# Kernel tuning notes

Measured on AMD Instinct MI355X. Metric: run time of the kernel, lower is better.

Reference implementation:

```python
import jax, jax.numpy as jnp
import numpy as np

B, T, DIM, H, HD = 1, 4096, 1024, 8, 128
ATTN_SCALE = 0.12


def _rms_norm(x):
    # F.rms_norm with default eps = finfo(dtype).eps, no learned weight
    eps = jnp.asarray(jnp.finfo(x.dtype).eps, x.dtype)
    return x * jax.lax.rsqrt(jnp.mean(x * x, axis=-1, keepdims=True) + eps)


def _rotary(x):
    # x: [B, T, H, D]; half-rotary: last D/2 freqs are zero (identity)
    t, d = x.shape[1], x.shape[-1]
    freqs = (1.0 / 1024.0) ** jnp.linspace(0.0, 1.0, d // 4, dtype=jnp.float32)
    freqs = jnp.concatenate([freqs, jnp.zeros(d // 4, dtype=jnp.float32)])
    theta = jnp.arange(t, dtype=jnp.float32)[:, None] * freqs[None, :]  # [T, D/2]
    cos = jnp.cos(theta)[None, :, None, :]
    sin = jnp.sin(theta)[None, :, None, :]
    x1, x2 = jnp.split(x.astype(jnp.float32), 2, axis=-1)
    y = jnp.concatenate([x1 * cos + x2 * sin, -x1 * sin + x2 * cos], axis=-1)
    return y.astype(x.dtype)


def setup_inputs() -> dict:
    key = jax.random.key(0)
    k1, k2, k3, k4, k5 = jax.random.split(key, 5)
    std = 0.5 * DIM ** -0.5
    bound = (3.0 ** 0.5) * std
    x = jax.random.normal(k1, (B, T, DIM), dtype=jnp.float32)
    ve = jax.random.normal(k2, (B, T, DIM), dtype=jnp.float32)
    qkv_w = jax.random.uniform(k3, (3, H * HD, DIM), dtype=jnp.float32,
                               minval=-bound, maxval=bound)
    lambdas = jnp.array([0.5, 0.5], dtype=jnp.float32)
    # c_proj is zero-initialized in the source; use small random weights so the
    # output (and gradients) are non-trivial for correctness testing
    c_proj_w = jax.random.normal(k4, (DIM, H * HD), dtype=jnp.float32) * 0.02
    docs = jnp.sort(jax.random.randint(k5, (T,), 0, 8, dtype=jnp.int32))
    return {"x": x, "ve": ve, "qkv_w": qkv_w, "lambdas": lambdas,
            "c_proj_w": c_proj_w, "docs": docs}


def reference(x, ve, qkv_w, lambdas, c_proj_w, docs):
    b, t, _ = x.shape
    w = qkv_w.reshape(3 * H * HD, -1)              # [3*hdim, dim]
    qkv = (x @ w.T).reshape(b, t, 3, H, HD)        # chunk(3, dim=-2) == axis 2 here
    q, k, v = qkv[:, :, 0], qkv[:, :, 1], qkv[:, :, 2]
    q, k = _rms_norm(q), _rms_norm(k)
    q, k = _rotary(q), _rotary(k)
    v = lambdas[0] * v + lambdas[1] * ve.reshape(v.shape)
    # doc-causal mask: attend within the same document, causally
    i = jnp.arange(t)
    mask = (i[:, None] >= i[None, :]) & (docs[:, None] == docs[None, :])  # [T, T]
    scores = jnp.einsum('bihd,bjhd->bhij', q, k) * ATTN_SCALE
    scores = jnp.where(mask[None, None], scores, -jnp.inf)
    p = jax.nn.softmax(scores, axis=-1)
    y = jnp.einsum('bhij,bjhd->bihd', p, v).reshape(b, t, H * HD)
    return y @ c_proj_w.T
```

## Files before the change

### kernel.cpp

```cpp
#include <hip/hip_runtime.h>
#include <hip/hip_bf16.h>
#include <cstdint>

typedef __attribute__((ext_vector_type(8))) short sh8;
typedef __attribute__((ext_vector_type(4))) float f4;

#define T_SEQ 4096
#define DIMN  1024
#define NH    8
#define HDIM  128
#define NQKV  3072
#define ATTN_SCALE 0.12f

__device__ __forceinline__ ushort f2bf(float x) {
  __hip_bfloat16 b = __float2bfloat16(x);
  return *reinterpret_cast<ushort*>(&b);
}
__device__ __forceinline__ float bf2f(ushort u) {
  uint v = ((uint)u) << 16;
  float f;
  __builtin_memcpy(&f, &v, 4);
  return f;
}

#define GLDS16(g, l) \
  __builtin_amdgcn_global_load_lds((const __attribute__((address_space(1))) void*)(g), \
                                   (__attribute__((address_space(3))) void*)(l), 16, 0, 0)

__global__ void k_f32_to_bf16(const float* __restrict__ in, ushort* __restrict__ out, int n4) {
  int i = blockIdx.x * blockDim.x + threadIdx.x;
  if (i >= n4) return;
  float4 v = reinterpret_cast<const float4*>(in)[i];
  ushort4 o;
  o.x = f2bf(v.x); o.y = f2bf(v.y); o.z = f2bf(v.z); o.w = f2bf(v.w);
  reinterpret_cast<ushort4*>(out)[i] = o;
}

__global__ void k_docstart(const int* __restrict__ docs, int* __restrict__ dstart, int n) {
  int i = blockIdx.x * blockDim.x + threadIdx.x;
  if (i >= n) return;
  int d = docs[i];
  int lo = 0, hi = i;
  while (lo < hi) { int mid = (lo + hi) >> 1; if (docs[mid] < d) lo = mid + 1; else hi = mid; }
  dstart[i] = lo;
}

template <typename OT>
__global__ __launch_bounds__(256) void k_gemm(const ushort* __restrict__ A,
                                              const ushort* __restrict__ B,
                                              OT* __restrict__ C, int N, int K) {
  __shared__ ushort As[128 * 64];
  __shared__ ushort Bs[128 * 64];
  const int tid = threadIdx.x;
  const int lane = tid & 63;
  const int wave = tid >> 6;
  const int lr = lane & 15, lg = lane >> 4;
  const int wr = wave >> 1, wc = wave & 1;
  const int m0 = blockIdx.y * 128, n0 = blockIdx.x * 128;

  const f4 fzero = {0.f, 0.f, 0.f, 0.f};
  f4 acc[4][4];
#pragma unroll
  for (int i = 0; i < 4; ++i)
#pragma unroll
    for (int j = 0; j < 4; ++j) acc[i][j] = fzero;

  const int srow_base = wave * 8 + (lane >> 3);
  const int scg = lane & 7;

  for (int k0 = 0; k0 < K; k0 += 64) {
    __syncthreads();
#pragma unroll
    for (int i = 0; i < 4; ++i) {
      const int row = i * 32 + srow_base;
      const int cgl = scg ^ (row & 7);
      GLDS16(A + (size_t)(m0 + row) * K + k0 + cgl * 8, &As[i * 2048 + wave * 512]);
      GLDS16(B + (size_t)(n0 + row) * K + k0 + cgl * 8, &Bs[i * 2048 + wave * 512]);
    }
    __syncthreads();

#pragma unroll
    for (int kk = 0; kk < 2; ++kk) {
      sh8 af[4], bfv[4];
#pragma unroll
      for (int mt = 0; mt < 4; ++mt) {
        const int row = wr * 64 + mt * 16 + lr;
        af[mt] = *reinterpret_cast<const sh8*>(&As[row * 64 + (((kk * 4 + lg) ^ (row & 7)) * 8)]);
      }
#pragma unroll
      for (int nt = 0; nt < 4; ++nt) {
        const int row = wc * 64 + nt * 16 + lr;
        bfv[nt] = *reinterpret_cast<const sh8*>(&Bs[row * 64 + (((kk * 4 + lg) ^ (row & 7)) * 8)]);
      }
#pragma unroll
      for (int mt = 0; mt < 4; ++mt)
#pragma unroll
        for (int nt = 0; nt < 4; ++nt)
          acc[mt][nt] = __builtin_amdgcn_mfma_f32_16x16x32_bf16(af[mt], bfv[nt], acc[mt][nt], 0, 0, 0);
    }
  }

#pragma unroll
  for (int mt = 0; mt < 4; ++mt)
#pragma unroll
    for (int nt = 0; nt < 4; ++nt) {
      const int gcol = n0 + wc * 64 + nt * 16 + lr;
#pragma unroll
      for (int r = 0; r < 4; ++r) {
        const int grow = m0 + wr * 64 + mt * 16 + lg * 4 + r;
        float v = acc[mt][nt][r];
        if constexpr (sizeof(OT) == 2)
          C[(size_t)grow * N + gcol] = (OT)f2bf(v);
        else
          C[(size_t)grow * N + gcol] = (OT)v;
      }
    }
}

__global__ __launch_bounds__(64) void k_fuse(const ushort* __restrict__ qkvb,
                                             const float* __restrict__ ve,
                                             const float* __restrict__ lam,
                                             ushort* __restrict__ qh, ushort* __restrict__ kh,
                                             ushort* __restrict__ vh) {
  const int bid = blockIdx.x;
  const int t = bid >> 3, h = bid & 7;
  const int l = threadIdx.x;
  const ushort* base = qkvb + (size_t)t * NQKV + h * HDIM + 2 * l;
  uint qu = *reinterpret_cast<const uint*>(base);
  uint ku = *reinterpret_cast<const uint*>(base + 1024);
  uint vu = *reinterpret_cast<const uint*>(base + 2048);
  float q0 = bf2f((ushort)qu), q1 = bf2f((ushort)(qu >> 16));
  float k0 = bf2f((ushort)ku), k1 = bf2f((ushort)(ku >> 16));
  float v0 = bf2f((ushort)vu), v1 = bf2f((ushort)(vu >> 16));
  float sq = q0 * q0 + q1 * q1, sk = k0 * k0 + k1 * k1;
#pragma unroll
  for (int m = 1; m < 64; m <<= 1) { sq += __shfl_xor(sq, m); sk += __shfl_xor(sk, m); }
  const float eps = 1.1920928955078125e-07f;
  float rq = rsqrtf(sq * (1.f / 128.f) + eps);
  float rk = rsqrtf(sk * (1.f / 128.f) + eps);
  q0 *= rq; q1 *= rq; k0 *= rk; k1 *= rk;
  float c0 = 1.f, s0 = 0.f, c1 = 1.f, s1 = 0.f;
  if ((l & 31) < 16) {
    const int f0 = 2 * (l & 31);
    float fr0 = exp2f(-10.f * (float)f0 * (1.f / 31.f));
    float fr1 = exp2f(-10.f * (float)(f0 + 1) * (1.f / 31.f));
    sincosf((float)t * fr0, &s0, &c0);
    sincosf((float)t * fr1, &s1, &c1);
  }
  float qx0 = __shfl_xor(q0, 32), qx1 = __shfl_xor(q1, 32);
  float kx0 = __shfl_xor(k0, 32), kx1 = __shfl_xor(k1, 32);
  const float sgn = (l < 32) ? 1.f : -1.f;
  float qr0 = q0 * c0 + sgn * qx0 * s0;
  float qr1 = q1 * c1 + sgn * qx1 * s1;
  float kr0 = k0 * c0 + sgn * kx0 * s0;
  float kr1 = k1 * c1 + sgn * kx1 * s1;
  const float l0 = lam[0], l1 = lam[1];
  float2 vev = *reinterpret_cast<const float2*>(ve + (size_t)t * DIMN + h * HDIM + 2 * l);
  float vr0 = l0 * v0 + l1 * vev.x;
  float vr1 = l0 * v1 + l1 * vev.y;
  const size_t o = ((size_t)h * T_SEQ + t) * HDIM + 2 * l;
  *reinterpret_cast<uint*>(qh + o) = (uint)f2bf(qr0) | ((uint)f2bf(qr1) << 16);
  *reinterpret_cast<uint*>(kh + o) = (uint)f2bf(kr0) | ((uint)f2bf(kr1) << 16);
  *reinterpret_cast<uint*>(vh + o) = (uint)f2bf(vr0) | ((uint)f2bf(vr1) << 16);
}

__global__ __launch_bounds__(256) void k_vt(const ushort* __restrict__ vh, ushort* __restrict__ vt) {
  const int tb = blockIdx.x, db = blockIdx.y, h = blockIdx.z;
  __shared__ ushort L[64][68];
  const int tid = threadIdx.x;
  const int t0 = tb * 64, d0 = db * 64;
  const size_t ib = ((size_t)h * T_SEQ + t0) * HDIM + d0;
#pragma unroll
  for (int p = 0; p < 4; ++p) {
    const int row = p * 16 + (tid >> 4);
    const int c4 = (tid & 15) * 4;
    ushort4 v = *reinterpret_cast<const ushort4*>(vh + ib + (size_t)row * HDIM + c4);
    *reinterpret_cast<ushort4*>(&L[row][c4]) = v;
  }
  __syncthreads();
  const size_t ob = ((size_t)h * HDIM + d0) * T_SEQ + t0;
#pragma unroll
  for (int p = 0; p < 4; ++p) {
    const int drow = p * 16 + (tid >> 4);
    const int t4 = (tid & 15) * 4;
    ushort4 v;
    v.x = L[t4 + 0][drow]; v.y = L[t4 + 1][drow];
    v.z = L[t4 + 2][drow]; v.w = L[t4 + 3][drow];
    *reinterpret_cast<ushort4*>(vt + ob + (size_t)drow * T_SEQ + t4) = v;
  }
}

__global__ __launch_bounds__(256) void k_attn(const ushort* __restrict__ qh,
                                              const ushort* __restrict__ kh,
                                              const ushort* __restrict__ vt,
                                              const int* __restrict__ doc_start,
                                              ushort* __restrict__ y) {
  const int h  = blockIdx.x;
  const int qb = blockIdx.y;
  const int q0 = qb * 64;
  const int tid  = threadIdx.x;
  const int wave = tid >> 6;
  const int lane = tid & 63;
  const int lr = lane & 15, lg = lane >> 4;

  __shared__ ushort Ks[2][64 * 128];
  __shared__ ushort Vs[2][128 * 64];
  __shared__ ushort Ps[4][16 * 64];

  const ushort* Kg = kh + (size_t)h * T_SEQ * HDIM;
  const ushort* Vg = vt + (size_t)h * HDIM * T_SEQ;

  const int i_me = q0 + wave * 16 + lr;
  sh8 qf[4];
  {
    const ushort* qp = qh + ((size_t)h * T_SEQ + i_me) * HDIM + lg * 8;
#pragma unroll
    for (int c = 0; c < 4; ++c) qf[c] = *reinterpret_cast<const sh8*>(qp + c * 32);
  }
  const int ds_me = doc_start[i_me];
  const int ds_hi = doc_start[q0 + 63];
  const int kb0   = doc_start[q0] >> 6;

  const f4 fzero = {0.f, 0.f, 0.f, 0.f};
  f4 o_acc[8];
#pragma unroll
  for (int i = 0; i < 8; ++i) o_acc[i] = fzero;
  float m_me = -1e30f, l_me = 0.f;

  auto STAGE = [&](int b, int k0) {
#pragma unroll
    for (int p = 0; p < 4; ++p) {
      const int c = p * 256 + tid;
      const int row = c >> 4, cc = c & 15;
      GLDS16(Kg + (size_t)(k0 + row) * HDIM + (cc ^ (row & 7)) * 8,
             &Ks[b][(p * 256 + wave * 64) * 8]);
    }
#pragma unroll
    for (int p = 0; p < 4; ++p) {
      const int c = p * 256 + tid;
      const int d = c >> 3, cc = c & 7;
      GLDS16(Vg + (size_t)d * T_SEQ + k0 + (cc ^ (d & 7)) * 8,
             &Vs[b][(p * 256 + wave * 64) * 8]);
    }
  };

  int cur = 0;
  STAGE(0, kb0 * 64);

  const int sw = (lr & 7) << 4;

  for (int kb = kb0; kb <= qb; ++kb) {
    const int k0 = kb * 64;
    __syncthreads();
    if (kb < qb) STAGE(cur ^ 1, k0 + 64);

    const char* Kb = (const char*)&Ks[cur][0];
    const char* Vb = (const char*)&Vs[cur][0];
    char* Pw = (char*)&Ps[wave][0];

    f4 sacc[4];
#pragma unroll
    for (int jt = 0; jt < 4; ++jt) sacc[jt] = fzero;
#pragma unroll
    for (int jt = 0; jt < 4; ++jt)
#pragma unroll
      for (int c = 0; c < 4; ++c) {
        sh8 kf = *reinterpret_cast<const sh8*>(Kb + (jt * 16 + lr) * 256 + ((c * 64 + lg * 16) ^ sw));
        sacc[jt] = __builtin_amdgcn_mfma_f32_16x16x32_bf16(kf, qf[c], sacc[jt], 0, 0, 0);
      }

    const bool fullblk = (kb < qb) && (ds_hi <= k0);
    float p[4][4];
#pragma unroll
    for (int jt = 0; jt < 4; ++jt)
#pragma unroll
      for (int r = 0; r < 4; ++r) {
        float s = sacc[jt][r] * ATTN_SCALE;
        const int j = k0 + jt * 16 + lg * 4 + r;
        bool valid = fullblk || ((j <= i_me) && (j >= ds_me));
        p[jt][r] = valid ? s : -1e30f;
      }
    float tm = -1e30f;
#pragma unroll
    for (int jt = 0; jt < 4; ++jt) {
      float a = fmaxf(p[jt][0], p[jt][1]), b = fmaxf(p[jt][2], p[jt][3]);
      tm = fmaxf(tm, fmaxf(a, b));
    }
    tm = fmaxf(tm, __shfl_xor(tm, 16));
    tm = fmaxf(tm, __shfl_xor(tm, 32));
    const float mnew = fmaxf(m_me, tm);
    const float sc = __expf(m_me - mnew);
    m_me = mnew;
    float rs = 0.f;
#pragma unroll
    for (int jt = 0; jt < 4; ++jt)
#pragma unroll
      for (int r = 0; r < 4; ++r) {
        float pv = __expf(p[jt][r] - mnew);
        p[jt][r] = pv;
        rs += pv;
      }
    rs += __shfl_xor(rs, 16);
    rs += __shfl_xor(rs, 32);
    l_me = l_me * sc + rs;

#pragma unroll
    for (int jt = 0; jt < 4; ++jt) {
      uint2 u;
      u.x = (uint)f2bf(p[jt][0]) | ((uint)f2bf(p[jt][1]) << 16);
      u.y = (uint)f2bf(p[jt][2]) | ((uint)f2bf(p[jt][3]) << 16);
      *reinterpret_cast<uint2*>(Pw + lr * 128 + ((jt * 32 + lg * 8) ^ sw)) = u;
    }

    float sco[4];
#pragma unroll
    for (int rr = 0; rr < 4; ++rr) sco[rr] = __shfl(sc, lg * 4 + rr);
#pragma unroll
    for (int dt = 0; dt < 8; ++dt)
#pragma unroll
      for (int rr = 0; rr < 4; ++rr) o_acc[dt][rr] *= sco[rr];

#pragma unroll
    for (int ks = 0; ks < 2; ++ks) {
      sh8 pa = *reinterpret_cast<const sh8*>(Pw + lr * 128 + ((ks * 64 + lg * 16) ^ sw));
#pragma unroll
      for (int dt = 0; dt < 8; ++dt) {
        sh8 vf = *reinterpret_cast<const sh8*>(Vb + (dt * 16 + lr) * 128 + ((ks * 64 + lg * 16) ^ sw));
        o_acc[dt] = __builtin_amdgcn_mfma_f32_16x16x32_bf16(pa, vf, o_acc[dt], 0, 0, 0);
      }
    }

    __builtin_amdgcn_s_barrier();
    cur ^= 1;
  }

  float lo[4];
#pragma unroll
  for (int rr = 0; rr < 4; ++rr) lo[rr] = __shfl(l_me, lg * 4 + rr);
#pragma unroll
  for (int dt = 0; dt < 8; ++dt)
#pragma unroll
    for (int rr = 0; rr < 4; ++rr) {
      const int trow = q0 + wave * 16 + lg * 4 + rr;
      y[(size_t)trow * DIMN + h * HDIM + dt * 16 + lr] = f2bf(o_acc[dt][rr] / lo[rr]);
    }
}

extern "C" void kernel_launch(void* const* d_in, const int* in_sizes, int n_in,
                              void* d_out, int out_size, void* d_ws, size_t ws_size,
                              hipStream_t stream) {
  const float* x    = (const float*)d_in[0];
  const float* ve   = (const float*)d_in[1];
  const float* qkvw = (const float*)d_in[2];
  const float* lam  = (const float*)d_in[3];
  const float* cpw  = (const float*)d_in[4];
  const int*   docs = (const int*)d_in[5];
  float* out = (float*)d_out;
  char* ws = (char*)d_ws;

  ushort* qkvb = (ushort*)(ws);
  ushort* xb   = (ushort*)(ws + (24ull << 20));
  ushort* wb   = (ushort*)(ws + (32ull << 20));
  ushort* cb   = (ushort*)(ws + (38ull << 20));
  ushort* qh   = (ushort*)(ws + (40ull << 20));
  ushort* kh   = (ushort*)(ws + (48ull << 20));
  ushort* vh   = (ushort*)(ws + (56ull << 20));
  ushort* vt   = (ushort*)(ws + (64ull << 20));
  ushort* yb   = (ushort*)(ws + (72ull << 20));
  int*  dstart = (int*)(ws + (80ull << 20));

  k_f32_to_bf16<<<(T_SEQ * DIMN / 4) / 256, 256, 0, stream>>>(x, xb, T_SEQ * DIMN / 4);
  k_f32_to_bf16<<<(NQKV * DIMN / 4) / 256, 256, 0, stream>>>(qkvw, wb, NQKV * DIMN / 4);
  k_f32_to_bf16<<<(DIMN * DIMN / 4) / 256, 256, 0, stream>>>(cpw, cb, DIMN * DIMN / 4);

  k_gemm<ushort><<<dim3(NQKV / 128, T_SEQ / 128), 256, 0, stream>>>(xb, wb, qkvb, NQKV, DIMN);

  k_fuse<<<T_SEQ * NH, 64, 0, stream>>>(qkvb, ve, lam, qh, kh, vh);
  k_docstart<<<T_SEQ / 256, 256, 0, stream>>>(docs, dstart, T_SEQ);
  k_vt<<<dim3(T_SEQ / 64, HDIM / 64, NH), 256, 0, stream>>>(vh, vt);

  k_attn<<<dim3(NH, T_SEQ / 64), 256, 0, stream>>>(qh, kh, vt, dstart, yb);

  k_gemm<float><<<dim3(DIMN / 128, T_SEQ / 128), 256, 0, stream>>>(yb, cb, out, DIMN, DIMN);
}
```

Before: 117.9 us.

## Merge prep kernels, add triple-buffered GEMM with larger tiles, batch fuse blocks

```diff
diff --git a/kernel.cpp b/kernel.cpp
--- a/kernel.cpp
+++ b/kernel.cpp
@@ -27,104 +27,163 @@
   __builtin_amdgcn_global_load_lds((const __attribute__((address_space(1))) void*)(g), \
                                    (__attribute__((address_space(3))) void*)(l), 16, 0, 0)
 
-__global__ void k_f32_to_bf16(const float* __restrict__ in, ushort* __restrict__ out, int n4) {
-  int i = blockIdx.x * blockDim.x + threadIdx.x;
-  if (i >= n4) return;
-  float4 v = reinterpret_cast<const float4*>(in)[i];
-  ushort4 o;
-  o.x = f2bf(v.x); o.y = f2bf(v.y); o.z = f2bf(v.z); o.w = f2bf(v.w);
-  reinterpret_cast<ushort4*>(out)[i] = o;
-}
-
-__global__ void k_docstart(const int* __restrict__ docs, int* __restrict__ dstart, int n) {
-  int i = blockIdx.x * blockDim.x + threadIdx.x;
-  if (i >= n) return;
-  int d = docs[i];
-  int lo = 0, hi = i;
-  while (lo < hi) { int mid = (lo + hi) >> 1; if (docs[mid] < d) lo = mid + 1; else hi = mid; }
-  dstart[i] = lo;
-}
-
-template <typename OT>
-__global__ __launch_bounds__(256) void k_gemm(const ushort* __restrict__ A,
-                                              const ushort* __restrict__ B,
-                                              OT* __restrict__ C, int N, int K) {
-  __shared__ ushort As[128 * 64];
-  __shared__ ushort Bs[128 * 64];
+template <int N>
+__device__ __forceinline__ void wait_vmcnt() {
+  if constexpr (N == 0)      asm volatile("s_waitcnt vmcnt(0)" ::: "memory");
+  else if constexpr (N == 4) asm volatile("s_waitcnt vmcnt(4)" ::: "memory");
+  else if constexpr (N == 6) asm volatile("s_waitcnt vmcnt(6)" ::: "memory");
+  else if constexpr (N == 8) asm volatile("s_waitcnt vmcnt(8)" ::: "memory");
+  __builtin_amdgcn_sched_barrier(0);
+}
+
+__global__ __launch_bounds__(256) void k_prep(const float* __restrict__ x,
+                                              const float* __restrict__ qw,
+                                              const float* __restrict__ cw,
+                                              ushort* __restrict__ xb, ushort* __restrict__ wb,
+                                              ushort* __restrict__ cbuf,
+                                              const int* __restrict__ docs, int* __restrict__ dstart) {
+  const int b = blockIdx.x;
+  if (b < 8192) {
+    const int i = b * 256 + threadIdx.x;
+    const float* src;
+    ushort* dst;
+    int j;
+    if (i < 1048576)       { src = x;  dst = xb;   j = i; }
+    else if (i < 1835008)  { src = qw; dst = wb;   j = i - 1048576; }
+    else                   { src = cw; dst = cbuf; j = i - 1835008; }
+    float4 v = reinterpret_cast<const float4*>(src)[j];
+    ushort4 o;
+    o.x = f2bf(v.x); o.y = f2bf(v.y); o.z = f2bf(v.z); o.w = f2bf(v.w);
+    reinterpret_cast<ushort4*>(dst)[j] = o;
+  } else {
+    const int i = (b - 8192) * 256 + threadIdx.x;
+    if (i < T_SEQ) {
+      int d = docs[i];
+      int lo = 0, hi = i;
+      while (lo < hi) { int mid = (lo + hi) >> 1; if (docs[mid] < d) lo = mid + 1; else hi = mid; }
+      dstart[i] = lo;
+    }
+  }
+}
+
+template <int BM, int BN, int WM, int WN, typename OT>
+__global__ __launch_bounds__(WM * WN * 64) void k_gemm2(const ushort* __restrict__ A,
+                                                        const ushort* __restrict__ B,
+                                                        OT* __restrict__ C,
+                                                        int N, int K, int gx) {
+  constexpr int NW  = WM * WN;
+  constexpr int CHA = BM * 4;
+  constexpr int CHT = (BM + BN) * 4;
+  constexpr int LPW = CHT / (NW * 64);
+  constexpr int TILEB = (BM + BN) * 64;
+  constexpr int MF = BM / WM / 16;
+  constexpr int NF = BN / WN / 16;
+
+  __shared__ __attribute__((aligned(16))) char lds[3 * TILEB];
+
   const int tid = threadIdx.x;
   const int lane = tid & 63;
-  const int wave = tid >> 6;
+  const int w = tid >> 6;
   const int lr = lane & 15, lg = lane >> 4;
-  const int wr = wave >> 1, wc = wave & 1;
-  const int m0 = blockIdx.y * 128, n0 = blockIdx.x * 128;
+  const int wm = w / WN, wn = w % WN;
+
+  const int nwg = gridDim.x;
+  const int nb = (blockIdx.x & 7) * (nwg >> 3) + (blockIdx.x >> 3);
+  const int m0 = (nb / gx) * BM;
+  const int n0 = (nb % gx) * BN;
 
   const f4 fzero = {0.f, 0.f, 0.f, 0.f};
-  f4 acc[4][4];
-#pragma unroll
-  for (int i = 0; i < 4; ++i)
-#pragma unroll
-    for (int j = 0; j < 4; ++j) acc[i][j] = fzero;
-
-  const int srow_base = wave * 8 + (lane >> 3);
-  const int scg = lane & 7;
-
-  for (int k0 = 0; k0 < K; k0 += 64) {
-    __syncthreads();
-#pragma unroll
-    for (int i = 0; i < 4; ++i) {
-      const int row = i * 32 + srow_base;
-      const int cgl = scg ^ (row & 7);
-      GLDS16(A + (size_t)(m0 + row) * K + k0 + cgl * 8, &As[i * 2048 + wave * 512]);
-      GLDS16(B + (size_t)(n0 + row) * K + k0 + cgl * 8, &Bs[i * 2048 + wave * 512]);
-    }
-    __syncthreads();
-
-#pragma unroll
-    for (int kk = 0; kk < 2; ++kk) {
-      sh8 af[4], bfv[4];
-#pragma unroll
-      for (int mt = 0; mt < 4; ++mt) {
-        const int row = wr * 64 + mt * 16 + lr;
-        af[mt] = *reinterpret_cast<const sh8*>(&As[row * 64 + (((kk * 4 + lg) ^ (row & 7)) * 8)]);
-      }
-#pragma unroll
-      for (int nt = 0; nt < 4; ++nt) {
-        const int row = wc * 64 + nt * 16 + lr;
-        bfv[nt] = *reinterpret_cast<const sh8*>(&Bs[row * 64 + (((kk * 4 + lg) ^ (row & 7)) * 8)]);
-      }
-#pragma unroll
-      for (int mt = 0; mt < 4; ++mt)
-#pragma unroll
-        for (int nt = 0; nt < 4; ++nt)
-          acc[mt][nt] = __builtin_amdgcn_mfma_f32_16x16x32_bf16(af[mt], bfv[nt], acc[mt][nt], 0, 0, 0);
-    }
-  }
-
-#pragma unroll
-  for (int mt = 0; mt < 4; ++mt)
-#pragma unroll
-    for (int nt = 0; nt < 4; ++nt) {
-      const int gcol = n0 + wc * 64 + nt * 16 + lr;
+  f4 acc[MF][NF];
+#pragma unroll
+  for (int i = 0; i < MF; ++i)
+#pragma unroll
+    for (int j = 0; j < NF; ++j) acc[i][j] = fzero;
+
+  const int NT = K >> 5;
+
+  auto STAGE = [&](int t, int buf) {
+    const int k0 = t << 5;
+#pragma unroll
+    for (int l = 0; l < LPW; ++l) {
+      const int cb = (l * NW + w) * 64;
+      const int ch = cb + lane;
+      const ushort* src;
+      if (ch < CHA) {
+        const int row = ch >> 2;
+        const int cs = (ch & 3) ^ ((row >> 1) & 3);
+        src = A + (size_t)(m0 + row) * K + k0 + cs * 8;
+      } else {
+        const int c2 = ch - CHA;
+        const int row = c2 >> 2;
+        const int cs = (c2 & 3) ^ ((row >> 1) & 3);
+        src = B + (size_t)(n0 + row) * K + k0 + cs * 8;
+      }
+      GLDS16(src, lds + buf * TILEB + cb * 16);
+    }
+  };
+
+  STAGE(0, 0);
+  STAGE(1, 1);
+  wait_vmcnt<LPW>();
+  __builtin_amdgcn_s_barrier();
+
+  const int sw4 = (lr >> 1) & 3;
+  int bufc = 0;
+
+  for (int t = 0; t < NT; ++t) {
+    const bool more = (t + 2) < NT;
+    if (more) STAGE(t + 2, bufc == 0 ? 2 : (bufc == 1 ? 0 : 1));
+
+    const char* bb = lds + bufc * TILEB;
+    sh8 af[MF], bf[NF];
+#pragma unroll
+    for (int mt = 0; mt < MF; ++mt) {
+      const int row = wm * (BM / WM) + mt * 16 + lr;
+      af[mt] = *reinterpret_cast<const sh8*>(bb + (row * 4 + (lg ^ sw4)) * 16);
+    }
+#pragma unroll
+    for (int nt = 0; nt < NF; ++nt) {
+      const int row = wn * (BN / WN) + nt * 16 + lr;
+      bf[nt] = *reinterpret_cast<const sh8*>(bb + (CHA + row * 4 + (lg ^ sw4)) * 16);
+    }
+    __builtin_amdgcn_s_setprio(1);
+#pragma unroll
+    for (int mt = 0; mt < MF; ++mt)
+#pragma unroll
+      for (int nt = 0; nt < NF; ++nt)
+        acc[mt][nt] = __builtin_amdgcn_mfma_f32_16x16x32_bf16(af[mt], bf[nt], acc[mt][nt], 0, 0, 0);
+    __builtin_amdgcn_s_setprio(0);
+
+    if (more) wait_vmcnt<LPW>();
+    else      wait_vmcnt<0>();
+    __builtin_amdgcn_s_barrier();
+    bufc = bufc == 2 ? 0 : bufc + 1;
+  }
+
+#pragma unroll
+  for (int mt = 0; mt < MF; ++mt)
+#pragma unroll
+    for (int nt = 0; nt < NF; ++nt) {
+      const int gcol = n0 + wn * (BN / WN) + nt * 16 + lr;
 #pragma unroll
       for (int r = 0; r < 4; ++r) {
-        const int grow = m0 + wr * 64 + mt * 16 + lg * 4 + r;
-        float v = acc[mt][nt][r];
+        const int grow = m0 + wm * (BM / WM) + mt * 16 + lg * 4 + r;
         if constexpr (sizeof(OT) == 2)
-          C[(size_t)grow * N + gcol] = (OT)f2bf(v);
+          C[(size_t)grow * N + gcol] = (OT)f2bf(acc[mt][nt][r]);
         else
-          C[(size_t)grow * N + gcol] = (OT)v;
-      }
-    }
-}
-
-__global__ __launch_bounds__(64) void k_fuse(const ushort* __restrict__ qkvb,
-                                             const float* __restrict__ ve,
-                                             const float* __restrict__ lam,
-                                             ushort* __restrict__ qh, ushort* __restrict__ kh,
-                                             ushort* __restrict__ vh) {
-  const int bid = blockIdx.x;
-  const int t = bid >> 3, h = bid & 7;
-  const int l = threadIdx.x;
+          C[(size_t)grow * N + gcol] = (OT)acc[mt][nt][r];
+      }
+    }
+}
+
+__global__ __launch_bounds__(256) void k_fuse(const ushort* __restrict__ qkvb,
+                                              const float* __restrict__ ve,
+                                              const float* __restrict__ lam,
+                                              ushort* __restrict__ qh, ushort* __restrict__ kh,
+                                              ushort* __restrict__ vh) {
+  const int pair = blockIdx.x * 4 + (threadIdx.x >> 6);
+  const int t = pair >> 3, h = pair & 7;
+  const int l = threadIdx.x & 63;
   const ushort* base = qkvb + (size_t)t * NQKV + h * HDIM + 2 * l;
   uint qu = *reinterpret_cast<const uint*>(base);
   uint ku = *reinterpret_cast<const uint*>(base + 1024);
@@ -369,17 +428,14 @@
   ushort* yb   = (ushort*)(ws + (72ull << 20));
   int*  dstart = (int*)(ws + (80ull << 20));
 
-  k_f32_to_bf16<<<(T_SEQ * DIMN / 4) / 256, 256, 0, stream>>>(x, xb, T_SEQ * DIMN / 4);
-  k_f32_to_bf16<<<(NQKV * DIMN / 4) / 256, 256, 0, stream>>>(qkvw, wb, NQKV * DIMN / 4);
-  k_f32_to_bf16<<<(DIMN * DIMN / 4) / 256, 256, 0, stream>>>(cpw, cb, DIMN * DIMN / 4);
-
-  k_gemm<ushort><<<dim3(NQKV / 128, T_SEQ / 128), 256, 0, stream>>>(xb, wb, qkvb, NQKV, DIMN);
-
-  k_fuse<<<T_SEQ * NH, 64, 0, stream>>>(qkvb, ve, lam, qh, kh, vh);
-  k_docstart<<<T_SEQ / 256, 256, 0, stream>>>(docs, dstart, T_SEQ);
+  k_prep<<<8192 + 16, 256, 0, stream>>>(x, qkvw, cpw, xb, wb, cb, docs, dstart);
+
+  k_gemm2<256, 128, 2, 2, ushort><<<384, 256, 0, stream>>>(xb, wb, qkvb, NQKV, DIMN, NQKV / 128);
+
+  k_fuse<<<T_SEQ * NH / 4, 256, 0, stream>>>(qkvb, ve, lam, qh, kh, vh);
   k_vt<<<dim3(T_SEQ / 64, HDIM / 64, NH), 256, 0, stream>>>(vh, vt);
 
   k_attn<<<dim3(NH, T_SEQ / 64), 256, 0, stream>>>(qh, kh, vt, dstart, yb);
 
-  k_gemm<float><<<dim3(DIMN / 128, T_SEQ / 128), 256, 0, stream>>>(yb, cb, out, DIMN, DIMN);
-}
+  k_gemm2<128, 128, 2, 2, float><<<256, 256, 0, stream>>>(yb, cb, out, DIMN, DIMN, DIMN / 128);
+}
```

Measured after the change: 117.7 us. About the same (-0.1%).
